# Kernel optimization log

Hardware: AMD Instinct MI355X
Metric: run time of the kernel (lower is better)

Reference implementation:

```python
import jax, jax.numpy as jnp
import numpy as np

# DualAttention dims
D_MODEL = 1024
H_SA = 8          # self-attention heads
H_RA = 8          # relational-attention heads
TOTAL_H = H_SA + H_RA
HEAD_DIM = D_MODEL // TOTAL_H   # 64
KEY_DIM = HEAD_DIM              # 64
N_REL = 8
REL_PROJ = HEAD_DIM * H_RA // N_REL  # 64
B, S = 2, 2048


def apply_rope(x, cos, sin):
    # x: [b, s, h, d]; cos/sin: [s, d//2]. Pairs are (0,1),(2,3),... as in
    # llama-style apply_rotary_emb (reshape(..., -1, 2).unbind(-1)).
    xr, xi = x[..., 0::2], x[..., 1::2]
    c = cos[None, :, None, :]
    s_ = sin[None, :, None, :]
    out = jnp.stack([xr * c - xi * s_, xr * s_ + xi * c], axis=-1)
    return out.reshape(x.shape)


def setup_inputs() -> dict:
    key = jax.random.key(0)
    ks = jax.random.split(key, 16)
    def w(k, shape):
        return jax.random.normal(k, shape, jnp.float32) * 0.02
    x = jax.random.normal(ks[0], (B, S, D_MODEL), jnp.float32)
    symbols = jax.random.normal(ks[1], (B, S, D_MODEL), jnp.float32)
    # real RoPE tables
    pos = np.arange(S, dtype=np.float32)[:, None]
    inv = 1.0 / (10000.0 ** (np.arange(0, KEY_DIM, 2, dtype=np.float32) / KEY_DIM))
    ang = pos * inv[None, :]
    freqs_cos = jnp.asarray(np.cos(ang), jnp.float32)
    freqs_sin = jnp.asarray(np.sin(ang), jnp.float32)
    return dict(
        x=x, symbols=symbols, freqs_cos=freqs_cos, freqs_sin=freqs_sin,
        # self-attention branch (torch Linear weights: [out, in])
        wq_sa=w(ks[2], (H_SA * KEY_DIM, D_MODEL)),
        wk_sa=w(ks[3], (H_SA * KEY_DIM, D_MODEL)),
        wv_sa=w(ks[4], (H_SA * HEAD_DIM, D_MODEL)),
        wo_sa=w(ks[5], (H_SA * HEAD_DIM, H_SA * HEAD_DIM)),
        # relational-attention branch
        wq_attn=w(ks[6], (H_RA * KEY_DIM, D_MODEL)),
        wk_attn=w(ks[7], (H_RA * KEY_DIM, D_MODEL)),
        wq_rel=w(ks[8], (N_REL * REL_PROJ, D_MODEL)),
        wk_rel=w(ks[9], (N_REL * REL_PROJ, D_MODEL)),
        wr=w(ks[10], (H_RA, HEAD_DIM, N_REL)),
        wv_ra=w(ks[11], (H_RA * HEAD_DIM, D_MODEL)),
        wo_ra=w(ks[12], (H_RA * HEAD_DIM, H_RA * HEAD_DIM)),
    )


def reference(x, symbols, freqs_cos, freqs_sin,
              wq_sa, wk_sa, wv_sa, wo_sa,
              wq_attn, wk_attn, wq_rel, wk_rel, wr, wv_ra, wo_ra):
    b, s, _ = x.shape
    attn_scale = 1.0 / np.sqrt(HEAD_DIM).astype(np.float32)
    rel_scale = 1.0 / np.sqrt(REL_PROJ).astype(np.float32)
    causal = jnp.tril(jnp.ones((s, s), dtype=bool))
    neg = jnp.finfo(x.dtype).min

    def heads(t, h, d):
        return t.reshape(b, s, h, d)

    # ---- self-attention branch (causal SDPA with RoPE) ----
    q = apply_rope(heads(x @ wq_sa.T, H_SA, KEY_DIM), freqs_cos, freqs_sin)
    k = apply_rope(heads(x @ wk_sa.T, H_SA, KEY_DIM), freqs_cos, freqs_sin)
    v = heads(x @ wv_sa.T, H_SA, HEAD_DIM)
    scores = jnp.einsum('bihd,bjhd->bhij', q, k) * attn_scale
    a = jax.nn.softmax(jnp.where(causal, scores, neg), axis=-1)
    sa_out = jnp.einsum('bhij,bjhd->bihd', a, v).reshape(b, s, H_SA * HEAD_DIM) @ wo_sa.T

    # ---- relational-attention branch ----
    # attention scores (softmax selection), with RoPE
    qa = apply_rope(heads(x @ wq_attn.T, H_RA, KEY_DIM), freqs_cos, freqs_sin)
    ka = apply_rope(heads(x @ wk_attn.T, H_RA, KEY_DIM), freqs_cos, freqs_sin)
    ra_scores = jnp.einsum('bihd,bjhd->bhij', qa, ka) * attn_scale
    alpha = jax.nn.softmax(jnp.where(causal, ra_scores, neg), axis=-1)
    # relations r(x_i, x_j) in R^{N_REL} (identity rel_activation)
    qr = heads(x @ wq_rel.T, N_REL, REL_PROJ)
    kr = heads(x @ wk_rel.T, N_REL, REL_PROJ)
    rel = jnp.einsum('birp,bjrp->brij', qr, kr) * rel_scale  # [b, R, i, j]
    # symbol values: wv applied to retrieved symbols
    sv = heads(symbols @ wv_ra.T, H_RA, HEAD_DIM)
    attended_sym = jnp.einsum('bhij,bjhd->bihd', alpha, sv)          # [b, i, h, d]
    attended_rel = jnp.einsum('bhij,brij->bihr', alpha, rel)         # [b, i, h, R]
    rel_out = jnp.einsum('bihr,hdr->bihd', attended_rel, wr)
    ra_out = (attended_sym + rel_out).reshape(b, s, H_RA * HEAD_DIM) @ wo_ra.T

    # DualAttention: concat branch outputs along feature dim -> [b, s, d_model]
    return jnp.concatenate([sa_out, ra_out], axis=-1)
```

## Files before the change

### kernel.cpp

```cpp
#include <hip/hip_runtime.h>

#define B_   2
#define S_   2048
#define H_   8
#define D_   64
#define DM_  1024
#define PJ_  512
#define NT_  32
#define NTRI 528
#define NCHK2 40

typedef short bf16x8 __attribute__((ext_vector_type(8)));
typedef float f32x4 __attribute__((ext_vector_type(4)));

__device__ __forceinline__ float bf2f(unsigned int u) {
  return __uint_as_float(u << 16);
}
__device__ __forceinline__ unsigned short f2bf(float f) {
  unsigned int u = __float_as_uint(f);
  u += 0x7fffu + ((u >> 16) & 1u);
  return (unsigned short)(u >> 16);
}
__device__ __forceinline__ unsigned int cvtpk_bf16(float lo, float hi) {
  unsigned int r;
  asm("v_cvt_pk_bf16_f32 %0, %1, %2" : "=v"(r) : "v"(lo), "v"(hi));
  return r;
}
__device__ __forceinline__ bf16x8 u4_to_bf(uint4 v) {
  union { uint4 a; bf16x8 b; } u; u.a = v; return u.b;
}

__device__ __forceinline__ void glds16(const unsigned short* g, unsigned short* l) {
  __builtin_amdgcn_global_load_lds(
      (const __attribute__((address_space(1))) void*)g,
      (__attribute__((address_space(3))) void*)l, 16, 0, 0);
}

struct CvtJobs {
  const float*    src[12];
  unsigned short* dst[12];
  int             n4[12];
};

__global__ __launch_bounds__(256) void cvt_many(CvtJobs J) {
  const int j = blockIdx.y;
  const int i = blockIdx.x * 256 + threadIdx.x;
  if (i >= J.n4[j]) return;
  const float4 v = ((const float4*)J.src[j])[i];
  ushort4 o;
  o.x = f2bf(v.x); o.y = f2bf(v.y); o.z = f2bf(v.z); o.w = f2bf(v.w);
  ((ushort4*)J.dst[j])[i] = o;
}

__device__ __forceinline__
void gemm128_glds(const unsigned short* __restrict__ A, int m0,
                  const unsigned short* __restrict__ Wb,
                  unsigned short* __restrict__ Cb, int ldc, int KD,
                  unsigned short* As, unsigned short* Bs)
{
  const int tid = threadIdx.x;
  const int wv = tid >> 6, lane = tid & 63;
  const int r15 = lane & 15, quad = lane >> 4;
  const int wm = (wv >> 1) * 64, wn = (wv & 1) * 64;
  f32x4 acc[4][4];
#pragma unroll
  for (int i = 0; i < 4; ++i)
#pragma unroll
    for (int j = 0; j < 4; ++j) acc[i][j] = (f32x4){0.f, 0.f, 0.f, 0.f};

  const int srow = wv * 16 + (lane >> 2);
  const int scol = ((lane & 3) ^ ((lane >> 3) & 3)) * 8;
  const unsigned short* gaA0 = A + (size_t)(m0 + srow) * KD + scol;
  const unsigned short* gaA1 = gaA0 + (size_t)64 * KD;
  const unsigned short* gaB0 = Wb + (size_t)srow * KD + scol;
  const unsigned short* gaB1 = gaB0 + (size_t)64 * KD;
  unsigned short* ldsA0 = As + wv * 512;
  unsigned short* ldsA1 = As + 2048 + wv * 512;
  unsigned short* ldsB0 = Bs + wv * 512;
  unsigned short* ldsB1 = Bs + 2048 + wv * 512;
  const int rxor = (r15 >> 1) & 3;

  for (int kk = 0; kk < KD; kk += 32) {
    __syncthreads();
    glds16(gaA0 + kk, ldsA0);
    glds16(gaA1 + kk, ldsA1);
    glds16(gaB0 + kk, ldsB0);
    glds16(gaB1 + kk, ldsB1);
    __syncthreads();
    bf16x8 af[4], bf[4];
#pragma unroll
    for (int i = 0; i < 4; ++i)
      af[i] = *(const bf16x8*)(As + (wm + i * 16 + r15) * 32 + ((quad ^ rxor) << 3));
#pragma unroll
    for (int j = 0; j < 4; ++j)
      bf[j] = *(const bf16x8*)(Bs + (wn + j * 16 + r15) * 32 + ((quad ^ rxor) << 3));
#pragma unroll
    for (int i = 0; i < 4; ++i)
#pragma unroll
      for (int j = 0; j < 4; ++j)
        acc[i][j] = __builtin_amdgcn_mfma_f32_16x16x32_bf16(af[i], bf[j], acc[i][j], 0, 0, 0);
  }
#pragma unroll
  for (int i = 0; i < 4; ++i)
#pragma unroll
    for (int r = 0; r < 4; ++r) {
      unsigned short* cp = Cb + (size_t)(wm + i * 16 + quad * 4 + r) * ldc + wn + r15;
#pragma unroll
      for (int j = 0; j < 4; ++j) cp[j * 16] = f2bf(acc[i][j][r]);
    }
}

__global__ __launch_bounds__(256)
void proj_tiled(const unsigned short* __restrict__ XB,
                const unsigned short* __restrict__ SYB,
                const unsigned short* __restrict__ Wcat,
                unsigned short* __restrict__ Qbase,
                unsigned short* __restrict__ SV)
{
  __shared__ unsigned short As[128 * 32];
  __shared__ unsigned short Bs[128 * 32];
  const int m0 = blockIdx.x * 128;
  const int ny = blockIdx.y;
  const size_t NB = (size_t)B_ * S_ * PJ_;
  const unsigned short* A;
  const unsigned short* Wb;
  unsigned short* Cb;
  if (ny < 28) {
    const int n0 = ny * 128;
    A  = XB;
    Wb = Wcat + (size_t)n0 * DM_;
    Cb = Qbase + (size_t)(n0 >> 9) * NB + (size_t)m0 * PJ_ + (n0 & 511);
  } else {
    const int n0 = (ny - 28) * 128;
    A  = SYB;
    Wb = Wcat + (size_t)7 * PJ_ * DM_ + (size_t)n0 * DM_;
    Cb = SV + (size_t)m0 * PJ_ + n0;
  }
  gemm128_glds(A, m0, Wb, Cb, PJ_, DM_, As, Bs);
}

__global__ __launch_bounds__(256)
void out_tiled(const unsigned short* __restrict__ Asa,
               const unsigned short* __restrict__ Ara,
               const unsigned short* __restrict__ WOSA,
               const unsigned short* __restrict__ WORA,
               float* __restrict__ Out)
{
  __shared__ unsigned short As[128 * 40];
  __shared__ unsigned short Bs[64 * 40];
  const int m0 = blockIdx.x * 128;
  const int ny = blockIdx.y;
  const int n0 = (ny & 7) * 64;
  const unsigned short* A  = (ny < 8) ? Asa : Ara;
  const unsigned short* Wb = ((ny < 8) ? WOSA : WORA) + (size_t)n0 * PJ_;
  float* Cb = Out + (size_t)m0 * DM_ + ((ny < 8) ? 0 : 512) + n0;

  const int tid = threadIdx.x;
  const int wv = tid >> 6, lane = tid & 63;
  const int r15 = lane & 15, quad = lane >> 4;
  const int wm = wv * 32;
  f32x4 acc[2][4];
#pragma unroll
  for (int i = 0; i < 2; ++i)
#pragma unroll
    for (int j = 0; j < 4; ++j) acc[i][j] = (f32x4){0.f, 0.f, 0.f, 0.f};

  const int arow = tid >> 1, ac = (tid & 1) * 16;
  const int brow = tid >> 2, bc = (tid & 3) * 8;
  const unsigned short* ga = A + (size_t)(m0 + arow) * PJ_ + ac;
  const unsigned short* gb = Wb + (size_t)brow * PJ_ + bc;
  unsigned short* la = As + arow * 40 + ac;
  unsigned short* lb = Bs + brow * 40 + bc;

  for (int kk = 0; kk < PJ_; kk += 32) {
    __syncthreads();
    const uint4 a0 = *(const uint4*)(ga + kk);
    const uint4 a1 = *(const uint4*)(ga + kk + 8);
    const uint4 b0 = *(const uint4*)(gb + kk);
    *(uint4*)la       = a0;
    *(uint4*)(la + 8) = a1;
    *(uint4*)lb       = b0;
    __syncthreads();
    bf16x8 af[2], bf[4];
#pragma unroll
    for (int i = 0; i < 2; ++i)
      af[i] = *(const bf16x8*)(As + (wm + i * 16 + r15) * 40 + quad * 8);
#pragma unroll
    for (int j = 0; j < 4; ++j)
      bf[j] = *(const bf16x8*)(Bs + (j * 16 + r15) * 40 + quad * 8);
#pragma unroll
    for (int i = 0; i < 2; ++i)
#pragma unroll
      for (int j = 0; j < 4; ++j)
        acc[i][j] = __builtin_amdgcn_mfma_f32_16x16x32_bf16(af[i], bf[j], acc[i][j], 0, 0, 0);
  }
#pragma unroll
  for (int i = 0; i < 2; ++i)
#pragma unroll
    for (int r = 0; r < 4; ++r) {
      float* cp = Cb + (size_t)(wm + i * 16 + quad * 4 + r) * DM_ + r15;
#pragma unroll
      for (int j = 0; j < 4; ++j) cp[j * 16] = acc[i][j][r];
    }
}

__global__ __launch_bounds__(256)
void rel_rope(const unsigned short* __restrict__ QRg, const unsigned short* __restrict__ KRg,
              unsigned short* __restrict__ RelCF,
              unsigned short* __restrict__ Qp, unsigned short* __restrict__ Kp,
              unsigned short* __restrict__ QAp, unsigned short* __restrict__ KAp,
              const float* __restrict__ fcp, const float* __restrict__ fsp)
{
  __shared__ unsigned short As[128 * 72];
  __shared__ unsigned short Bs[128 * 72];
  const int t = blockIdx.x;
  int I = 0;
  while ((I + 1) * (I + 2) / 2 <= t) ++I;
  const int J = t - I * (I + 1) / 2;
  const int rr = blockIdx.y & 7, b = blockIdx.y >> 3;
  const int tid = threadIdx.x;
  const int wv = tid >> 6, lane = tid & 63;
  const int r15 = lane & 15, quad = lane >> 4;

  const int srow = tid >> 1, c32 = (tid & 1) * 32;
  const unsigned short* ga = QRg + (size_t)(b * S_ + I * 128 + srow) * PJ_ + rr * 64 + c32;
  const unsigned short* gb = KRg + (size_t)(b * S_ + J * 128 + srow) * PJ_ + rr * 64 + c32;
  unsigned short* la = As + srow * 72 + c32;
  unsigned short* lb = Bs + srow * 72 + c32;
#pragma unroll
  for (int q = 0; q < 4; ++q) {
    *(uint4*)(la + q * 8) = *(const uint4*)(ga + q * 8);
    *(uint4*)(lb + q * 8) = *(const uint4*)(gb + q * 8);
  }
  __syncthreads();

  const int wm = (wv >> 1) * 64, wn = (wv & 1) * 64;
  const int it64 = 2 * I + (wv >> 1), jt64 = 2 * J + (wv & 1);
  if (jt64 <= it64) {
    f32x4 acc[4][4];
#pragma unroll
    for (int a = 0; a < 4; ++a)
#pragma unroll
      for (int bq = 0; bq < 4; ++bq) acc[a][bq] = (f32x4){0.f, 0.f, 0.f, 0.f};
#pragma unroll
    for (int k0 = 0; k0 < 2; ++k0) {
      bf16x8 af[4], bf[4];
#pragma unroll
      for (int i = 0; i < 4; ++i)
        af[i] = *(const bf16x8*)(As + (wm + i * 16 + r15) * 72 + quad * 8 + k0 * 32);
#pragma unroll
      for (int j = 0; j < 4; ++j)
        bf[j] = *(const bf16x8*)(Bs + (wn + j * 16 + r15) * 72 + quad * 8 + k0 * 32);
#pragma unroll
      for (int a = 0; a < 4; ++a)
#pragma unroll
        for (int bq = 0; bq < 4; ++bq)
          acc[a][bq] = __builtin_amdgcn_mfma_f32_16x16x32_bf16(bf[a], af[bq], acc[a][bq], 0, 0, 0);
    }
    unsigned short* out = RelCF + ((size_t)(b * 8 + rr) * NTRI + (size_t)it64 * (it64 + 1) / 2 + jt64) * 4096;
#pragma unroll
    for (int bq = 0; bq < 4; ++bq) {
      unsigned short tmp[16];
#pragma unroll
      for (int a = 0; a < 4; ++a)
#pragma unroll
        for (int r = 0; r < 4; ++r)
          tmp[a * 4 + r] = f2bf(acc[a][bq][r] * 0.125f);
      unsigned short* op = out + (size_t)bq * 1024 + (size_t)lane * 8;
      *(uint4*)op         = *(const uint4*)tmp;
      *(uint4*)(op + 512) = *(const uint4*)(tmp + 8);
    }
  }

  const int bid = (int)blockIdx.y * 136 + (int)blockIdx.x;
  const int gt = bid * 256 + tid;
#pragma unroll
  for (int k = 0; k < 2; ++k) {
    const int i = gt * 2 + k;
    if (i >= 4 * 262144) continue;
    const int tn = i >> 18;
    const int r2 = i & 262143;
    unsigned short* P = (tn == 0) ? Qp : (tn == 1) ? Kp : (tn == 2) ? QAp : KAp;
    const int b2 = r2 >> 17;
    const int s2 = (r2 >> 6) & 2047;
    const int c8 = (r2 & 63) * 8;
    const int ci0 = (c8 & 63) >> 1;
    const size_t off2 = ((size_t)(b2 * S_ + s2)) * PJ_ + c8;
    uint4 v = *(const uint4*)(P + off2);
    unsigned int u[4] = {v.x, v.y, v.z, v.w};
    unsigned int o[4];
#pragma unroll
    for (int q = 0; q < 4; ++q) {
      const float xr = __uint_as_float(u[q] << 16);
      const float xi = __uint_as_float(u[q] & 0xffff0000u);
      const float cs = fcp[s2 * 32 + ci0 + q];
      const float sn = fsp[s2 * 32 + ci0 + q];
      const unsigned short lo = f2bf(xr * cs - xi * sn);
      const unsigned short hi = f2bf(xr * sn + xi * cs);
      o[q] = (unsigned int)lo | ((unsigned int)hi << 16);
    }
    uint4 ov; ov.x = o[0]; ov.y = o[1]; ov.z = o[2]; ov.w = o[3];
    *(uint4*)(P + off2) = ov;
  }
}

__global__ __launch_bounds__(512)
void flash_part(const unsigned short* __restrict__ Qsa, const unsigned short* __restrict__ Ksa,
                const unsigned short* __restrict__ Vsa,
                const unsigned short* __restrict__ Qra, const unsigned short* __restrict__ Kra,
                const unsigned short* __restrict__ SVra,
                const unsigned short* __restrict__ RelCF,
                unsigned short* __restrict__ PoP, float* __restrict__ lP,
                float* __restrict__ arpP)
{
  __shared__ unsigned short Ks[2][2][64][72];
  __shared__ unsigned short Vt[2][2][64][72];
  const int x = NCHK2 - 1 - (int)blockIdx.x;
  int a, c;
  if (x < 4)       { a = x;                 c = 0; }
  else if (x < 12) { a = 4 + ((x - 4) >> 1);  c = (x - 4) & 1; }
  else if (x < 24) { a = 8 + (x - 12) / 3;    c = (x - 12) % 3; }
  else             { a = 12 + ((x - 24) >> 2); c = (x - 24) & 3; }
  const int j0 = c * 8;
  const int jendF = 2 * a + 2;
  const int jend = (j0 + 8 < jendF) ? (j0 + 8) : jendF;
  const bool ra = (blockIdx.y >= 8);
  const int h = blockIdx.y & 7;
  const int b = blockIdx.z;
  const int chunkId = (b * 16 + (int)blockIdx.y) * NCHK2 + x;
  const unsigned short* Qg = ra ? Qra : Qsa;
  const unsigned short* Kg = ra ? Kra : Ksa;
  const unsigned short* Vg = ra ? SVra : Vsa;
  const int tid = threadIdx.x;
  const int wv = tid >> 6, lane = tid & 63;
  const int r15 = lane & 15, quad = lane >> 4;
  const size_t bh = (size_t)b * S_ * PJ_ + (size_t)h * D_;
  const size_t relStride = (size_t)NTRI * 4096;
  const int it_wave = 2 * a + (wv >> 2);
  const int gi = a * 128 + wv * 16 + r15;

  const int kr = tid >> 3, kc0 = (tid & 7) << 3;
  const unsigned short* kgp = Kg + bh + (size_t)kr * PJ_ + kc0;
  const unsigned short* vgp = Vg + bh + (size_t)lane * PJ_ + wv * 8;
  const int kcol = ((lane >> 2) & 3) * 8 + ((lane >> 4) & 1) * 4 + (lane & 3) + (lane >> 5) * 32;

  const unsigned short* qp = Qg + bh + (size_t)gi * PJ_ + quad * 8;
  const bf16x8 aq0 = *(const bf16x8*)qp;
  const bf16x8 aq1 = *(const bf16x8*)(qp + 32);

  const bf16x8 ones = (bf16x8)(short)0x3F80;

  f32x4 o_acc[4];
  f32x4 l_acc = (f32x4){0.f, 0.f, 0.f, 0.f};
  f32x4 accR[8];
#pragma unroll
  for (int n = 0; n < 4; ++n) o_acc[n] = (f32x4){0.f, 0.f, 0.f, 0.f};
#pragma unroll
  for (int rr = 0; rr < 8; ++rr) accR[rr] = (f32x4){0.f, 0.f, 0.f, 0.f};
  const size_t relTileBase = (size_t)(b * 8) * NTRI * 4096
                           + (size_t)(it_wave * (it_wave + 1)) / 2 * 4096
                           + (size_t)(wv & 3) * 1024 + (size_t)lane * 8;

  auto TILE = [&](int jtt, const unsigned short (*KsT)[72], const unsigned short (*VtT)[72]) {
    const bool dorel = ra && (jtt <= it_wave);
    const unsigned short* rtBase = RelCF + relTileBase + (size_t)jtt * 4096;
    uint4 pre[8];
    if (dorel) {
      const unsigned short* rt = rtBase;
#pragma unroll
      for (int q = 0; q < 4; ++q) {
        pre[2 * q]     = *(const uint4*)rt;
        pre[2 * q + 1] = *(const uint4*)(rt + 512);
        rt += relStride;
      }
    }
    f32x4 s[4];
#pragma unroll
    for (int n = 0; n < 4; ++n) s[n] = (f32x4){0.f, 0.f, 0.f, 0.f};
#pragma unroll
    for (int k0 = 0; k0 < 2; ++k0) {
      const bf16x8 bq = k0 ? aq1 : aq0;
#pragma unroll
      for (int n = 0; n < 4; ++n) {
        const bf16x8 kf = *(const bf16x8*)&KsT[n * 16 + r15][quad * 8 + k0 * 32];
        s[n] = __builtin_amdgcn_mfma_f32_16x16x32_bf16(kf, bq, s[n], 0, 0, 0);
      }
    }
    if (jtt >= it_wave) {
#pragma unroll
      for (int n = 0; n < 4; ++n)
#pragma unroll
        for (int r = 0; r < 4; ++r) {
          const bool ok = (jtt * 64 + n * 16 + quad * 4 + r <= gi);
          s[n][r] = ok ? exp2f(fmaf(s[n][r], 0.180336887f, -5.770780163f)) : 0.f;
        }
    } else {
#pragma unroll
      for (int n = 0; n < 4; ++n)
#pragma unroll
        for (int r = 0; r < 4; ++r)
          s[n][r] = exp2f(fmaf(s[n][r], 0.180336887f, -5.770780163f));
    }
    uint4 w0, w1;
    w0.x = cvtpk_bf16(s[0][0], s[0][1]); w0.y = cvtpk_bf16(s[0][2], s[0][3]);
    w0.z = cvtpk_bf16(s[1][0], s[1][1]); w0.w = cvtpk_bf16(s[1][2], s[1][3]);
    w1.x = cvtpk_bf16(s[2][0], s[2][1]); w1.y = cvtpk_bf16(s[2][2], s[2][3]);
    w1.z = cvtpk_bf16(s[3][0], s[3][1]); w1.w = cvtpk_bf16(s[3][2], s[3][3]);
    const bf16x8 pa0 = u4_to_bf(w0);
    const bf16x8 pa1 = u4_to_bf(w1);
    l_acc = __builtin_amdgcn_mfma_f32_16x16x32_bf16(pa0, ones, l_acc, 0, 0, 0);
    l_acc = __builtin_amdgcn_mfma_f32_16x16x32_bf16(pa1, ones, l_acc, 0, 0, 0);
    if (dorel) {
#pragma unroll
      for (int rr = 0; rr < 4; ++rr) {
        accR[rr] = __builtin_amdgcn_mfma_f32_16x16x32_bf16(pa0, u4_to_bf(pre[2 * rr]), accR[rr], 0, 0, 0);
        accR[rr] = __builtin_amdgcn_mfma_f32_16x16x32_bf16(pa1, u4_to_bf(pre[2 * rr + 1]), accR[rr], 0, 0, 0);
      }
    }
#pragma unroll
    for (int k0 = 0; k0 < 2; ++k0) {
      const bf16x8 pf = k0 ? pa1 : pa0;
#pragma unroll
      for (int n = 0; n < 4; ++n) {
        const bf16x8 vf = *(const bf16x8*)&VtT[n * 16 + r15][quad * 8 + k0 * 32];
        o_acc[n] = __builtin_amdgcn_mfma_f32_16x16x32_bf16(pf, vf, o_acc[n], 0, 0, 0);
      }
    }
    if (dorel) {
      const unsigned short* rt2 = rtBase + 4 * relStride;
#pragma unroll
      for (int rr = 4; rr < 8; ++rr) {
        const bf16x8 rb0 = *(const bf16x8*)rt2;
        const bf16x8 rb1 = *(const bf16x8*)(rt2 + 512);
        accR[rr] = __builtin_amdgcn_mfma_f32_16x16x32_bf16(pa0, rb0, accR[rr], 0, 0, 0);
        accR[rr] = __builtin_amdgcn_mfma_f32_16x16x32_bf16(pa1, rb1, accR[rr], 0, 0, 0);
        rt2 += relStride;
      }
    }
  };

  uint4 ka0, ka1, va0, va1;
  {
    const size_t jb0 = (size_t)j0 * 64 * PJ_;
    const size_t jb1 = (size_t)(j0 + 1) * 64 * PJ_;
    ka0 = *(const uint4*)(kgp + jb0);
    ka1 = *(const uint4*)(kgp + jb1);
    va0 = *(const uint4*)(vgp + jb0);
    va1 = *(const uint4*)(vgp + jb1);
  }
  int p = 0;
  {
    *(uint4*)&Ks[0][0][kr][kc0] = ka0;
    *(uint4*)&Ks[0][1][kr][kc0] = ka1;
    unsigned short t8[8];
    *(uint4*)t8 = va0;
#pragma unroll
    for (int m = 0; m < 8; ++m) Vt[0][0][wv * 8 + m][kcol] = t8[m];
    *(uint4*)t8 = va1;
#pragma unroll
    for (int m = 0; m < 8; ++m) Vt[0][1][wv * 8 + m][kcol] = t8[m];
  }
  __syncthreads();

  for (int jt = j0; jt < jend; jt += 2) {
    const bool more = (jt + 2 < jend);
    if (more) {
      const size_t jb0 = (size_t)(jt + 2) * 64 * PJ_;
      const size_t jb1 = (size_t)(jt + 3) * 64 * PJ_;
      ka0 = *(const uint4*)(kgp + jb0);
      ka1 = *(const uint4*)(kgp + jb1);
      va0 = *(const uint4*)(vgp + jb0);
      va1 = *(const uint4*)(vgp + jb1);
    }
    TILE(jt,     Ks[p][0], Vt[p][0]);
    TILE(jt + 1, Ks[p][1], Vt[p][1]);
    if (more) {
      const int q = p ^ 1;
      *(uint4*)&Ks[q][0][kr][kc0] = ka0;
      *(uint4*)&Ks[q][1][kr][kc0] = ka1;
      unsigned short t8[8];
      *(uint4*)t8 = va0;
#pragma unroll
      for (int m = 0; m < 8; ++m) Vt[q][0][wv * 8 + m][kcol] = t8[m];
      *(uint4*)t8 = va1;
#pragma unroll
      for (int m = 0; m < 8; ++m) Vt[q][1][wv * 8 + m][kcol] = t8[m];
      __syncthreads();
      p = q;
    }
  }
  unsigned short* po = PoP + (size_t)chunkId * 8192;
#pragma unroll
  for (int n = 0; n < 4; ++n)
#pragma unroll
    for (int r = 0; r < 4; ++r)
      po[(wv * 16 + quad * 4 + r) * 64 + n * 16 + r15] = f2bf(o_acc[n][r]);
  if (r15 == 0) {
#pragma unroll
    for (int r = 0; r < 4; ++r)
      lP[(size_t)chunkId * 128 + wv * 16 + quad * 4 + r] = l_acc[r];
  }
  if (ra && quad == (r15 >> 2)) {
    const int d3 = r15 & 3;
    float* ap = arpP + (size_t)chunkId * 1024 + (size_t)(wv * 16 + r15) * 8;
#pragma unroll
    for (int rr = 0; rr < 8; ++rr) {
      const f32x4 a4 = accR[rr];
      const float v = (d3 == 0) ? a4[0] : (d3 == 1) ? a4[1] : (d3 == 2) ? a4[2] : a4[3];
      ap[rr] = v;
    }
  }
}

__global__ __launch_bounds__(256)
void flash_merge(const unsigned short* __restrict__ PoP, const float* __restrict__ lP,
                 const float* __restrict__ arpP, const float* __restrict__ wrF,
                 unsigned short* __restrict__ Osa, unsigned short* __restrict__ Ora)
{
  const int it = blockIdx.x;
  const int hh = blockIdx.y;
  const int b  = blockIdx.z;
  const bool ra = (hh >= 8);
  const int h = hh & 7;
  const int a  = it >> 1;
  const int half = it & 1;
  const int nc = ((2 * a + 1) >> 3) + 1;
  int cb;
  if (a < 4)       cb = a;
  else if (a < 8)  cb = 4 + 2 * (a - 4);
  else if (a < 12) cb = 12 + 3 * (a - 8);
  else             cb = 24 + 4 * (a - 12);
  const int cid0 = (b * 16 + hh) * NCHK2 + cb;
  const int tid = threadIdx.x;
  const int row = tid >> 2;
  const int cg  = tid & 3;
  const int prow = half * 64 + row;

  float L = 0.f;
  for (int c = 0; c < nc; ++c) L += lP[(size_t)(cid0 + c) * 128 + prow];
  const float inv = 1.f / L;

  float o[16];
#pragma unroll
  for (int k = 0; k < 16; ++k) o[k] = 0.f;
  for (int c = 0; c < nc; ++c) {
    const unsigned short* pp = PoP + (size_t)(cid0 + c) * 8192 + prow * 64 + cg * 16;
    unsigned int u[8];
    *(uint4*)u       = *(const uint4*)pp;
    *(uint4*)(u + 4) = *(const uint4*)(pp + 8);
#pragma unroll
    for (int q = 0; q < 8; ++q) {
      o[2 * q]     += __uint_as_float(u[q] << 16);
      o[2 * q + 1] += __uint_as_float(u[q] & 0xffff0000u);
    }
  }
  if (ra) {
    float A[8];
#pragma unroll
    for (int rr = 0; rr < 8; ++rr) A[rr] = 0.f;
    for (int c = 0; c < nc; ++c) {
      const float* ap = arpP + (size_t)(cid0 + c) * 1024 + (size_t)prow * 8;
#pragma unroll
      for (int rr = 0; rr < 8; ++rr) A[rr] += ap[rr];
    }
#pragma unroll
    for (int k = 0; k < 16; ++k) {
      const float* wp = wrF + ((size_t)h * 64 + cg * 16 + k) * 8;
      float ro = 0.f;
#pragma unroll
      for (int rr = 0; rr < 8; ++rr) ro += A[rr] * wp[rr];
      o[k] += ro;
    }
  }
  const size_t bh = (size_t)b * S_ * PJ_ + (size_t)h * D_;
  unsigned short* op = (ra ? Ora : Osa) + bh + (size_t)(it * 64 + row) * PJ_ + cg * 16;
#pragma unroll
  for (int k = 0; k < 16; ++k) op[k] = f2bf(o[k] * inv);
}

extern "C" void kernel_launch(void* const* d_in, const int* in_sizes, int n_in,
                              void* d_out, int out_size, void* d_ws, size_t ws_size,
                              hipStream_t stream)
{
  (void)in_sizes; (void)n_in; (void)out_size; (void)ws_size;
  const float* x    = (const float*)d_in[0];
  const float* sym  = (const float*)d_in[1];
  const float* fc   = (const float*)d_in[2];
  const float* fs   = (const float*)d_in[3];
  const float* wqsa = (const float*)d_in[4];
  const float* wksa = (const float*)d_in[5];
  const float* wvsa = (const float*)d_in[6];
  const float* wosa = (const float*)d_in[7];
  const float* wqat = (const float*)d_in[8];
  const float* wkat = (const float*)d_in[9];
  const float* wqre = (const float*)d_in[10];
  const float* wkre = (const float*)d_in[11];
  const float* wr   = (const float*)d_in[12];
  const float* wvra = (const float*)d_in[13];
  const float* wora = (const float*)d_in[14];

  unsigned short* wsb = (unsigned short*)d_ws;
  const size_t NX = (size_t)B_ * S_ * DM_;
  const size_t NB = (size_t)B_ * S_ * PJ_;
  const size_t NW = (size_t)PJ_ * DM_;
  const size_t NO = (size_t)PJ_ * PJ_;
  const size_t NR = (size_t)B_ * 8 * NTRI * 4096;
  const size_t NCH = (size_t)B_ * 16 * NCHK2;

  size_t off = 0;
  unsigned short* XB   = wsb + off; off += NX;
  unsigned short* SYB  = wsb + off; off += NX;
  unsigned short* WB[8];
  for (int i = 0; i < 8; ++i) { WB[i] = wsb + off; off += NW; }
  unsigned short* WOSA = wsb + off; off += NO;
  unsigned short* WORA = wsb + off; off += NO;
  unsigned short* Q    = wsb + off; off += NB;
  unsigned short* K    = wsb + off; off += NB;
  unsigned short* V    = wsb + off; off += NB;
  unsigned short* QA   = wsb + off; off += NB;
  unsigned short* KA   = wsb + off; off += NB;
  unsigned short* QR   = wsb + off; off += NB;
  unsigned short* KR   = wsb + off; off += NB;
  unsigned short* SV   = wsb + off; off += NB;
  unsigned short* Asa  = wsb + off; off += NB;
  unsigned short* Ara  = wsb + off; off += NB;
  unsigned short* RelCF = wsb + off; off += NR;
  unsigned short* PoP  = XB;
  float* lP   = (float*)(wsb + off); off += NCH * 128 * 2;
  float* arpP = (float*)(wsb + off); off += NCH * 1024 * 2;

  CvtJobs cj;
  cj.src[0]  = x;    cj.dst[0]  = XB;    cj.n4[0]  = (int)(NX / 4);
  cj.src[1]  = sym;  cj.dst[1]  = SYB;   cj.n4[1]  = (int)(NX / 4);
  cj.src[2]  = wqsa; cj.dst[2]  = WB[0]; cj.n4[2]  = (int)(NW / 4);
  cj.src[3]  = wksa; cj.dst[3]  = WB[1]; cj.n4[3]  = (int)(NW / 4);
  cj.src[4]  = wvsa; cj.dst[4]  = WB[2]; cj.n4[4]  = (int)(NW / 4);
  cj.src[5]  = wqat; cj.dst[5]  = WB[3]; cj.n4[5]  = (int)(NW / 4);
  cj.src[6]  = wkat; cj.dst[6]  = WB[4]; cj.n4[6]  = (int)(NW / 4);
  cj.src[7]  = wqre; cj.dst[7]  = WB[5]; cj.n4[7]  = (int)(NW / 4);
  cj.src[8]  = wkre; cj.dst[8]  = WB[6]; cj.n4[8]  = (int)(NW / 4);
  cj.src[9]  = wvra; cj.dst[9]  = WB[7]; cj.n4[9]  = (int)(NW / 4);
  cj.src[10] = wosa; cj.dst[10] = WOSA;  cj.n4[10] = (int)(NO / 4);
  cj.src[11] = wora; cj.dst[11] = WORA;  cj.n4[11] = (int)(NO / 4);
  cvt_many<<<dim3(4096, 12), dim3(256), 0, stream>>>(cj);

  proj_tiled<<<dim3(32, 32), dim3(256), 0, stream>>>(XB, SYB, WB[0], Q, SV);
  rel_rope<<<dim3(136, 16), dim3(256), 0, stream>>>(QR, KR, RelCF, Q, K, QA, KA, fc, fs);
  flash_part<<<dim3(NCHK2, 16, B_), dim3(512), 0, stream>>>(
      Q, K, V, QA, KA, SV, RelCF, PoP, lP, arpP);
  flash_merge<<<dim3(NT_, 16, B_), dim3(256), 0, stream>>>(
      PoP, lP, arpP, wr, Asa, Ara);
  out_tiled<<<dim3(32, 16), dim3(256), 0, stream>>>(Asa, Ara, WOSA, WORA, (float*)d_out);
}
```

Before: 303.2 us.

## Load K fragments directly from global, skip fully-masked tiles, add MFMA priority hints

```diff
diff --git a/kernel.cpp b/kernel.cpp
--- a/kernel.cpp
+++ b/kernel.cpp
@@ -313,7 +313,6 @@
                 unsigned short* __restrict__ PoP, float* __restrict__ lP,
                 float* __restrict__ arpP)
 {
-  __shared__ unsigned short Ks[2][2][64][72];
   __shared__ unsigned short Vt[2][2][64][72];
   const int x = NCHK2 - 1 - (int)blockIdx.x;
   int a, c;
@@ -339,10 +338,9 @@
   const int it_wave = 2 * a + (wv >> 2);
   const int gi = a * 128 + wv * 16 + r15;
 
-  const int kr = tid >> 3, kc0 = (tid & 7) << 3;
-  const unsigned short* kgp = Kg + bh + (size_t)kr * PJ_ + kc0;
   const unsigned short* vgp = Vg + bh + (size_t)lane * PJ_ + wv * 8;
   const int kcol = ((lane >> 2) & 3) * 8 + ((lane >> 4) & 1) * 4 + (lane & 3) + (lane >> 5) * 32;
+  const unsigned short* kfb = Kg + bh + (size_t)r15 * PJ_ + quad * 8;
 
   const unsigned short* qp = Qg + bh + (size_t)gi * PJ_ + quad * 8;
   const bf16x8 aq0 = *(const bf16x8*)qp;
@@ -361,11 +359,11 @@
                            + (size_t)(it_wave * (it_wave + 1)) / 2 * 4096
                            + (size_t)(wv & 3) * 1024 + (size_t)lane * 8;
 
-  auto TILE = [&](int jtt, const unsigned short (*KsT)[72], const unsigned short (*VtT)[72]) {
-    const bool dorel = ra && (jtt <= it_wave);
+  auto TILE = [&](int jtt, const unsigned short (*VtT)[72]) {
+    if (jtt > it_wave) return;
     const unsigned short* rtBase = RelCF + relTileBase + (size_t)jtt * 4096;
     uint4 pre[8];
-    if (dorel) {
+    if (ra) {
       const unsigned short* rt = rtBase;
 #pragma unroll
       for (int q = 0; q < 4; ++q) {
@@ -374,19 +372,22 @@
         rt += relStride;
       }
     }
+    const unsigned short* kt = kfb + (size_t)jtt * 64 * PJ_;
     f32x4 s[4];
 #pragma unroll
     for (int n = 0; n < 4; ++n) s[n] = (f32x4){0.f, 0.f, 0.f, 0.f};
+    __builtin_amdgcn_s_setprio(1);
 #pragma unroll
     for (int k0 = 0; k0 < 2; ++k0) {
       const bf16x8 bq = k0 ? aq1 : aq0;
 #pragma unroll
       for (int n = 0; n < 4; ++n) {
-        const bf16x8 kf = *(const bf16x8*)&KsT[n * 16 + r15][quad * 8 + k0 * 32];
+        const bf16x8 kf = *(const bf16x8*)(kt + (size_t)(n * 16) * PJ_ + k0 * 32);
         s[n] = __builtin_amdgcn_mfma_f32_16x16x32_bf16(kf, bq, s[n], 0, 0, 0);
       }
     }
-    if (jtt >= it_wave) {
+    __builtin_amdgcn_s_setprio(0);
+    if (jtt == it_wave) {
 #pragma unroll
       for (int n = 0; n < 4; ++n)
 #pragma unroll
@@ -408,9 +409,10 @@
     w1.z = cvtpk_bf16(s[3][0], s[3][1]); w1.w = cvtpk_bf16(s[3][2], s[3][3]);
     const bf16x8 pa0 = u4_to_bf(w0);
     const bf16x8 pa1 = u4_to_bf(w1);
+    __builtin_amdgcn_s_setprio(1);
     l_acc = __builtin_amdgcn_mfma_f32_16x16x32_bf16(pa0, ones, l_acc, 0, 0, 0);
     l_acc = __builtin_amdgcn_mfma_f32_16x16x32_bf16(pa1, ones, l_acc, 0, 0, 0);
-    if (dorel) {
+    if (ra) {
 #pragma unroll
       for (int rr = 0; rr < 4; ++rr) {
         accR[rr] = __builtin_amdgcn_mfma_f32_16x16x32_bf16(pa0, u4_to_bf(pre[2 * rr]), accR[rr], 0, 0, 0);
@@ -426,7 +428,7 @@
         o_acc[n] = __builtin_amdgcn_mfma_f32_16x16x32_bf16(pf, vf, o_acc[n], 0, 0, 0);
       }
     }
-    if (dorel) {
+    if (ra) {
       const unsigned short* rt2 = rtBase + 4 * relStride;
 #pragma unroll
       for (int rr = 4; rr < 8; ++rr) {
@@ -437,21 +439,18 @@
         rt2 += relStride;
       }
     }
+    __builtin_amdgcn_s_setprio(0);
   };
 
-  uint4 ka0, ka1, va0, va1;
+  uint4 va0, va1;
   {
     const size_t jb0 = (size_t)j0 * 64 * PJ_;
     const size_t jb1 = (size_t)(j0 + 1) * 64 * PJ_;
-    ka0 = *(const uint4*)(kgp + jb0);
-    ka1 = *(const uint4*)(kgp + jb1);
     va0 = *(const uint4*)(vgp + jb0);
     va1 = *(const uint4*)(vgp + jb1);
   }
   int p = 0;
   {
-    *(uint4*)&Ks[0][0][kr][kc0] = ka0;
-    *(uint4*)&Ks[0][1][kr][kc0] = ka1;
     unsigned short t8[8];
     *(uint4*)t8 = va0;
 #pragma unroll
@@ -467,17 +466,13 @@
     if (more) {
       const size_t jb0 = (size_t)(jt + 2) * 64 * PJ_;
       const size_t jb1 = (size_t)(jt + 3) * 64 * PJ_;
-      ka0 = *(const uint4*)(kgp + jb0);
-      ka1 = *(const uint4*)(kgp + jb1);
       va0 = *(const uint4*)(vgp + jb0);
       va1 = *(const uint4*)(vgp + jb1);
     }
-    TILE(jt,     Ks[p][0], Vt[p][0]);
-    TILE(jt + 1, Ks[p][1], Vt[p][1]);
+    TILE(jt,     Vt[p][0]);
+    TILE(jt + 1, Vt[p][1]);
     if (more) {
       const int q = p ^ 1;
-      *(uint4*)&Ks[q][0][kr][kc0] = ka0;
-      *(uint4*)&Ks[q][1][kr][kc0] = ka1;
       unsigned short t8[8];
       *(uint4*)t8 = va0;
 #pragma unroll
```

Measured after the change: 353.5 us. 1.17x slower.
